# Performance work log

Hardware: AMD Instinct MI355X
Metric: run time of the kernel (lower is better)

## Reference

```python
import jax, jax.numpy as jnp
import numpy as np

CAPACITY_FACTOR = 1.0


def setup_inputs() -> dict:
    key = jax.random.key(0)
    k = jax.random.split(key, 6)
    N, E, M, V = 8192, 8, 1024, 4096
    s = 0.02
    return {
        "x": jax.random.normal(k[0], (N, M), jnp.float32),
        "wg": jax.random.normal(k[1], (E, M), jnp.float32) * s,
        "fc1": jax.random.normal(k[2], (E, M, V), jnp.float32) * s,
        "b1": jax.random.normal(k[3], (E, V), jnp.float32) * s,
        "fc2": jax.random.normal(k[4], (E, V, M), jnp.float32) * s,
        "b2": jax.random.normal(k[5], (E, M), jnp.float32) * s,
    }


def reference(x, wg, fc1, b1, fc2, b2):
    N, M = x.shape
    E = wg.shape[0]
    capacity = 2 * int(CAPACITY_FACTOR * ((N + E - 1) // E))  # Top2 capacity

    # ---- Top2 gating ----
    logits = x @ wg.T                                   # [N, E]
    gates = jax.nn.softmax(logits, axis=1)
    _, top2 = jax.lax.top_k(logits, 2)                  # [N, 2]
    i1, i2 = top2[:, 0], top2[:, 1]
    m1 = jax.nn.one_hot(i1, E, dtype=jnp.int32)         # [N, E]
    m2 = jax.nn.one_hot(i2, E, dtype=jnp.int32)
    g1 = jnp.sum(gates * m1, axis=1)                    # [N]
    g2 = jnp.sum(gates * m2, axis=1)

    # cumulative-sum capacity assignment (per expert slot index)
    loc1 = jnp.cumsum(m1, axis=0) - 1                   # [N, E]
    loc2 = jnp.cumsum(m2, axis=0) - 1 + jnp.sum(m1, axis=0, keepdims=True)
    m1c = m1 * (loc1 < capacity).astype(jnp.int32)
    m2c = m2 * (loc2 < capacity).astype(jnp.int32)
    loc1_s = jnp.sum(loc1 * m1c, axis=1)                # [N]
    loc2_s = jnp.sum(loc2 * m2c, axis=1)
    v1 = jnp.sum(m1c, axis=1)                           # 0/1 kept flags
    v2 = jnp.sum(m2c, axis=1)

    # aux load-balancing loss (fp32 branch of original)
    me = jnp.sum(gates, axis=0)
    ce = jnp.sum(m1c.astype(gates.dtype), axis=0)
    l_aux = jnp.sum(me * ce) * (E / (N * N))

    # ---- dispatch (scatter tokens into [E*C, M]) ----
    idx1 = jnp.where(v1 > 0, i1 * capacity + loc1_s, -1)
    idx2 = jnp.where(v2 > 0, i2 * capacity + loc2_s, -1)
    disp = jnp.zeros((E * capacity, M), x.dtype)
    disp = disp.at[idx1].add(x, mode="drop")
    disp = disp.at[idx2].add(x, mode="drop")

    # ---- fused FFN experts ----
    d = disp.reshape(E, capacity, M)
    h = jnp.einsum("ecm,emv->ecv", d, fc1) + b1[:, None, :]
    h = jax.nn.relu(h)
    y = jnp.einsum("ecv,evm->ecm", h, fc2) + b2[:, None, :]
    yf = y.reshape(E * capacity, M)

    # ---- combine (gather + gate-weighted sum) ----
    v1f = v1.astype(x.dtype)
    v2f = v2.astype(x.dtype)
    out = (g1 * v1f)[:, None] * yf[i1 * capacity + loc1_s] \
        + (g2 * v2f)[:, None] * yf[i2 * capacity + loc2_s]
    return out, l_aux
```

## Files before the change

kernel.cpp:

```cpp
#include <hip/hip_runtime.h>
#include <stdint.h>

typedef __attribute__((ext_vector_type(8))) short short8;
typedef __attribute__((ext_vector_type(4))) float f32x4;

#define N_TOK 8192
#define E_EXP 8
#define M_DIM 1024
#define V_DIM 4096
#define CAP   2048
#define SLOTS (E_EXP*CAP)

__device__ __forceinline__ unsigned short f2bf(float f){
  unsigned u = __float_as_uint(f);
  u += 0x7FFFu + ((u >> 16) & 1u);
  return (unsigned short)(u >> 16);
}

__device__ __forceinline__ void gload_lds16(const void* g, void* l){
  __builtin_amdgcn_global_load_lds(
    (const __attribute__((address_space(1))) void*)g,
    (__attribute__((address_space(3))) void*)l, 16, 0, 0);
}

__global__ __launch_bounds__(256) void routing_kernel(
    const float* __restrict__ x, const float* __restrict__ wg,
    float* __restrict__ gates, int* __restrict__ i1o, int* __restrict__ i2o,
    float* __restrict__ g1o, float* __restrict__ g2o)
{
  int wv = threadIdx.x >> 6, lane = threadIdx.x & 63;
  int n = blockIdx.x * 4 + wv;
  const float* xr = x + (size_t)n * M_DIM;
  double acc[8];
  #pragma unroll
  for (int e = 0; e < 8; e++) acc[e] = 0.0;
  for (int j = 0; j < M_DIM/64; j++){
    double xv = (double)xr[lane + j*64];
    #pragma unroll
    for (int e = 0; e < 8; e++) acc[e] += xv * (double)wg[e*M_DIM + lane + j*64];
  }
  #pragma unroll
  for (int off = 32; off > 0; off >>= 1){
    #pragma unroll
    for (int e = 0; e < 8; e++) acc[e] += __shfl_down(acc[e], off);
  }
  if (lane == 0){
    float lg[8], mx = -1e30f;
    #pragma unroll
    for (int e = 0; e < 8; e++){ lg[e] = (float)acc[e]; mx = fmaxf(mx, lg[e]); }
    float s = 0.f, gt[8];
    #pragma unroll
    for (int e = 0; e < 8; e++){ gt[e] = expf(lg[e] - mx); s += gt[e]; }
    float inv = 1.f / s;
    int i1 = 0;
    #pragma unroll
    for (int e = 1; e < 8; e++) if (lg[e] > lg[i1]) i1 = e;
    int i2 = (i1 == 0) ? 1 : 0;
    #pragma unroll
    for (int e = 0; e < 8; e++){ if (e == i1) continue; if (lg[e] > lg[i2]) i2 = e; }
    #pragma unroll
    for (int e = 0; e < 8; e++) gates[(size_t)n*8 + e] = gt[e] * inv;
    i1o[n] = i1; i2o[n] = i2;
    g1o[n] = gt[i1] * inv; g2o[n] = gt[i2] * inv;
  }
}

__global__ __launch_bounds__(1024) void scan_kernel(
    const int* __restrict__ i1, const int* __restrict__ i2,
    int* __restrict__ s1, int* __restrict__ s2, int* __restrict__ ce_out)
{
  __shared__ unsigned long long sc[4][1024];
  const int t = threadIdx.x;
  int e1l[8], e2l[8];
  unsigned long long c[4] = {0ull,0ull,0ull,0ull};
  #pragma unroll
  for (int k = 0; k < 8; k++){
    int a = i1[t*8+k]; e1l[k] = a; c[a>>2]       += 1ull << ((a&3)*16);
    int b = i2[t*8+k]; e2l[k] = b; c[2 + (b>>2)] += 1ull << ((b&3)*16);
  }
  #pragma unroll
  for (int i = 0; i < 4; i++) sc[i][t] = c[i];
  __syncthreads();
  for (int st = 1; st < 1024; st <<= 1){
    unsigned long long add[4];
    #pragma unroll
    for (int i = 0; i < 4; i++) add[i] = (t >= st) ? sc[i][t-st] : 0ull;
    __syncthreads();
    #pragma unroll
    for (int i = 0; i < 4; i++) if (t >= st) sc[i][t] += add[i];
    __syncthreads();
  }
  unsigned long long ex[4], tot[4];
  #pragma unroll
  for (int i = 0; i < 4; i++){ ex[i] = sc[i][t] - c[i]; tot[i] = sc[i][1023]; }
  int r1[8], r2[8], t1[8];
  #pragma unroll
  for (int e = 0; e < 8; e++){
    r1[e] = (int)((ex[e>>2]       >> ((e&3)*16)) & 0xFFFF);
    r2[e] = (int)((ex[2 + (e>>2)] >> ((e&3)*16)) & 0xFFFF);
    t1[e] = (int)((tot[e>>2]      >> ((e&3)*16)) & 0xFFFF);
  }
  #pragma unroll
  for (int k = 0; k < 8; k++){
    int n = t*8 + k;
    int a = e1l[k]; int loc1 = r1[a]++;
    s1[n] = (loc1 < CAP) ? (a*CAP + loc1) : -1;
    int b = e2l[k]; int loc2 = r2[b]++ + t1[b];
    s2[n] = (loc2 < CAP) ? (b*CAP + loc2) : -1;
  }
  if (t == 0){
    #pragma unroll
    for (int e = 0; e < 8; e++) ce_out[e] = (t1[e] < CAP) ? t1[e] : CAP;
  }
}

__global__ __launch_bounds__(1024) void laux_kernel(
    const float* __restrict__ gates, const int* __restrict__ ce, float* __restrict__ dst)
{
  __shared__ float red[1024];
  const int t = threadIdx.x;
  float part[8];
  #pragma unroll
  for (int e = 0; e < 8; e++) part[e] = 0.f;
  for (int k = 0; k < 8; k++){
    int n = t + k*1024;
    #pragma unroll
    for (int e = 0; e < 8; e++) part[e] += gates[(size_t)n*8 + e];
  }
  float laux = 0.f;
  for (int e = 0; e < 8; e++){
    red[t] = part[e];
    __syncthreads();
    for (int s = 512; s > 0; s >>= 1){ if (t < s) red[t] += red[t+s]; __syncthreads(); }
    if (t == 0) laux += red[0] * (float)ce[e];
    __syncthreads();
  }
  if (t == 0) dst[0] = laux * (float)(8.0/(8192.0*8192.0));
}

__global__ void build_droplist(const int* __restrict__ s1, const int* __restrict__ s2,
                               int* __restrict__ list, int* __restrict__ cnt)
{
  int lane = threadIdx.x;
  int base = 0;
  int a = s1[lane], b = s2[lane];
  for (int it = 0; it < N_TOK/64; it++){
    int na = 0, nb = 0;
    if (it + 1 < N_TOK/64){
      na = s1[(it+1)*64 + lane];
      nb = s2[(it+1)*64 + lane];
    }
    int n = it*64 + lane;
    bool f1 = (a == -1) || (a == SLOTS-1);
    unsigned long long m1 = __ballot(f1);
    if (f1) list[base + __popcll(m1 & ((1ull<<lane)-1))] = n;
    base += __popcll(m1);
    bool f2 = (b == -1) || (b == SLOTS-1);
    unsigned long long m2 = __ballot(f2);
    if (f2) list[base + __popcll(m2 & ((1ull<<lane)-1))] = n;
    base += __popcll(m2);
    a = na; b = nb;
  }
  if (lane == 0) *cnt = base;
}

__global__ void dropacc1_kernel(const float* __restrict__ x, const int* __restrict__ list,
                                const int* __restrict__ cnt, float* __restrict__ partial)
{
  int col = blockIdx.x*256 + threadIdx.x;
  int sl  = blockIdx.y;
  int c = *cnt;
  int per = (c + 15) >> 4;
  int lo = sl*per, hi = lo + per; if (hi > c) hi = c;
  float a = 0.f;
  for (int i = lo; i < hi; i++) a += x[(size_t)list[i]*M_DIM + col];
  partial[sl*M_DIM + col] = a;
}
__global__ void dropacc2_kernel(const float* __restrict__ partial, float* __restrict__ drow)
{
  int col = blockIdx.x*256 + threadIdx.x;
  float s = 0.f;
  #pragma unroll
  for (int j = 0; j < 16; j++) s += partial[j*M_DIM + col];
  drow[col] = s;
}

template<bool RELU>
__global__ __launch_bounds__(256) void fix_gemv(
    const float* __restrict__ vec, const float* __restrict__ W,
    const float* __restrict__ bias, float* __restrict__ outv, int K, int N)
{
  __shared__ float red[256];
  const int o = threadIdx.x & 15;
  const int c = threadIdx.x >> 4;
  const int n = blockIdx.x*16 + o;
  const int chunk = K >> 4;
  float a = 0.f;
  for (int k = c*chunk; k < (c+1)*chunk; k++) a += vec[k] * W[(size_t)k*N + n];
  red[threadIdx.x] = a;
  __syncthreads();
  if (c == 0){
    float s = 0.f;
    #pragma unroll
    for (int j = 0; j < 16; j++) s += red[o + j*16];
    s += bias[n];
    if (RELU) s = fmaxf(s, 0.f);
    outv[n] = s;
  }
}

__global__ void scatter_kernel(const float* __restrict__ x, const int* __restrict__ s1,
                               const int* __restrict__ s2, unsigned short* __restrict__ dispB,
                               int e0, int epb)
{
  int n = blockIdx.x, t = threadIdx.x;
  int a = s1[n], b = s2[n];
  int za = (a >= 0) ? (a >> 11) - e0 : -1;
  int zb = (b >= 0) ? (b >> 11) - e0 : -1;
  bool wa = (za >= 0) && (za < epb);
  bool wb = (zb >= 0) && (zb < epb);
  if (!wa && !wb) return;
  const float4 v = *(const float4*)(x + (size_t)n*M_DIM + t*4);
  ushort4 o;
  o.x = f2bf(v.x); o.y = f2bf(v.y); o.z = f2bf(v.z); o.w = f2bf(v.w);
  if (wa) *(ushort4*)(dispB + ((size_t)za*CAP + (a & (CAP-1)))*M_DIM + t*4) = o;
  if (wb) *(ushort4*)(dispB + ((size_t)zb*CAP + (b & (CAP-1)))*M_DIM + t*4) = o;
}

__global__ __launch_bounds__(256) void transpose_f32_bf16(
    const float* __restrict__ in, unsigned short* __restrict__ out,
    int R, int C, size_t estride)
{
  __shared__ float tile[32][33];
  const size_t eo = (size_t)blockIdx.z * estride;
  int c0 = blockIdx.x*32, r0 = blockIdx.y*32;
  int tx = threadIdx.x & 31, ty = threadIdx.x >> 5;
  #pragma unroll
  for (int j = 0; j < 4; j++)
    tile[ty + j*8][tx] = in[eo + (size_t)(r0 + ty + j*8)*C + (c0 + tx)];
  __syncthreads();
  #pragma unroll
  for (int j = 0; j < 4; j++)
    out[eo + (size_t)(c0 + ty + j*8)*R + (r0 + tx)] = f2bf(tile[tx][ty + j*8]);
}

template<bool RELU_BF16>
__global__ __launch_bounds__(512, 2) void gemm_tn(
    const unsigned short* __restrict__ A, size_t aE,
    const unsigned short* __restrict__ B, size_t bE,
    const float* __restrict__ bias, size_t biasE,
    void* __restrict__ outp, size_t oE, int K, int Ncols, int gx, int gy)
{
  __shared__ unsigned short As[2][2][128*64];
  __shared__ unsigned short Bs[2][2][128*64];
  const int nwg = gridDim.x;
  const int orig = blockIdx.x;
  const int wgid = (orig & 7) * (nwg >> 3) + (orig >> 3);
  const int z  = wgid / (gx*gy);
  const int rr = wgid - z*gx*gy;
  const int by = rr / gx, bx = rr - by*gx;

  const unsigned short* Ae = A + (size_t)z * aE;
  const unsigned short* Be = B + (size_t)z * bE;
  const float* be = bias + (size_t)z * biasE;
  const int row0 = by * 256;
  const int col0 = bx * 256;
  const int tid = threadIdx.x;
  const int lane = tid & 63, wv = tid >> 6;
  const int wr = wv >> 2, wc = wv & 3;
  const int frow = lane & 15, fq = lane >> 4;

  f32x4 acc[8][4];
  #pragma unroll
  for (int i = 0; i < 8; i++)
    #pragma unroll
    for (int j = 0; j < 4; j++) acc[i][j] = (f32x4){0.f,0.f,0.f,0.f};

  auto STAGE_A = [&](int buf, int half, int k0){
    #pragma unroll
    for (int i = 0; i < 2; i++){
      int cb = i*512 + wv*64;
      int c  = cb + lane;
      int r  = c >> 3, s = c & 7;
      gload_lds16(Ae + (size_t)(row0 + half*128 + r)*K + (k0 + ((s ^ (r & 7))*8)),
                  &As[buf][half][cb*8]);
    }
  };
  auto STAGE_B = [&](int buf, int half, int k0){
    #pragma unroll
    for (int i = 0; i < 2; i++){
      int cb = i*512 + wv*64;
      int c  = cb + lane;
      int r  = c >> 3, s = c & 7;
      gload_lds16(Be + (size_t)(col0 + half*128 + r)*K + (k0 + ((s ^ (r & 7))*8)),
                  &Bs[buf][half][cb*8]);
    }
  };

  short8 a[8], bA[4], bB[4];
  auto READ_A = [&](int buf, int fmb){
    #pragma unroll
    for (int fm = 0; fm < 4; fm++)
      #pragma unroll
      for (int ks = 0; ks < 2; ks++){
        int row = wr*128 + (fmb+fm)*16 + frow;
        int h = row >> 7, r = row & 127;
        int sl = (ks*4 + fq) ^ (r & 7);
        a[fm*2+ks] = *(const short8*)&As[buf][h][r*64 + sl*8];
      }
  };
  auto READ_B = [&](int buf, int fnb, short8* dst){
    #pragma unroll
    for (int fn = 0; fn < 2; fn++)
      #pragma unroll
      for (int ks = 0; ks < 2; ks++){
        int col = wc*64 + (fnb+fn)*16 + frow;
        int h = col >> 7, r = col & 127;
        int sl = (ks*4 + fq) ^ (r & 7);
        dst[fn*2+ks] = *(const short8*)&Bs[buf][h][r*64 + sl*8];
      }
  };
  auto MFMA16 = [&](int fmb, int fnb, short8* b){
    #pragma unroll
    for (int fm = 0; fm < 4; fm++)
      #pragma unroll
      for (int fn = 0; fn < 2; fn++)
        #pragma unroll
        for (int ks = 0; ks < 2; ks++)
          acc[fmb+fm][fnb+fn] =
            __builtin_amdgcn_mfma_f32_16x16x32_bf16(a[fm*2+ks], b[fn*2+ks], acc[fmb+fm][fnb+fn], 0, 0, 0);
  };

  const int nt = K >> 6;
  const int iters = nt >> 1;
  STAGE_A(0, 0, 0); STAGE_A(0, 1, 0);
  STAGE_B(0, 0, 0); STAGE_B(0, 1, 0);
  STAGE_B(1, 0, 64); STAGE_B(1, 1, 64);
  asm volatile("s_waitcnt vmcnt(4)" ::: "memory");
  __builtin_amdgcn_sched_barrier(0);
  __builtin_amdgcn_s_barrier();

  for (int t = 0; t < iters; ++t){
    const bool more = (t + 1 < iters);
    const int kO = (2*t+1)*64;
    const int kN = (2*t+2)*64;
    const int kL = (2*t+3)*64;

    READ_A(0, 0); READ_B(0, 0, bA);
    STAGE_A(1, 0, kO);
    __builtin_amdgcn_s_barrier();
    asm volatile("s_waitcnt lgkmcnt(0)" ::: "memory");
    __builtin_amdgcn_sched_barrier(0);
    __builtin_amdgcn_s_setprio(1); MFMA16(0, 0, bA); __builtin_amdgcn_s_setprio(0);
    __builtin_amdgcn_s_barrier();
    READ_B(0, 2, bB);
    STAGE_A(1, 1, kO);
    __builtin_amdgcn_s_barrier();
    asm volatile("s_waitcnt lgkmcnt(0)" ::: "memory");
    __builtin_amdgcn_sched_barrier(0);
    __builtin_amdgcn_s_setprio(1); MFMA16(0, 2, bB); __builtin_amdgcn_s_setprio(0);
    __builtin_amdgcn_s_barrier();
    READ_A(0, 4);
    if (more) STAGE_B(0, 0, kN);
    __builtin_amdgcn_s_barrier();
    asm volatile("s_waitcnt lgkmcnt(0)" ::: "memory");
    __builtin_amdgcn_sched_barrier(0);
    __builtin_amdgcn_s_setprio(1); MFMA16(4, 0, bA); __builtin_amdgcn_s_setprio(0);
    __builtin_amdgcn_s_barrier();
    if (more) STAGE_B(0, 1, kN);
    __builtin_amdgcn_s_barrier();
    asm volatile("s_waitcnt lgkmcnt(0)" ::: "memory");
    __builtin_amdgcn_sched_barrier(0);
    __builtin_amdgcn_s_setprio(1); MFMA16(4, 2, bB); __builtin_amdgcn_s_setprio(0);
    if (more) asm volatile("s_waitcnt vmcnt(4)" ::: "memory");
    else      asm volatile("s_waitcnt vmcnt(0)" ::: "memory");
    __builtin_amdgcn_sched_barrier(0);
    __builtin_amdgcn_s_barrier();

    READ_A(1, 0); READ_B(1, 0, bA);
    if (more) STAGE_A(0, 0, kN);
    __builtin_amdgcn_s_barrier();
    asm volatile("s_waitcnt lgkmcnt(0)" ::: "memory");
    __builtin_amdgcn_sched_barrier(0);
    __builtin_amdgcn_s_setprio(1); MFMA16(0, 0, bA); __builtin_amdgcn_s_setprio(0);
    __builtin_amdgcn_s_barrier();
    READ_B(1, 2, bB);
    if (more) STAGE_A(0, 1, kN);
    __builtin_amdgcn_s_barrier();
    asm volatile("s_waitcnt lgkmcnt(0)" ::: "memory");
    __builtin_amdgcn_sched_barrier(0);
    __builtin_amdgcn_s_setprio(1); MFMA16(0, 2, bB); __builtin_amdgcn_s_setprio(0);
    __builtin_amdgcn_s_barrier();
    READ_A(1, 4);
    if (more) STAGE_B(1, 0, kL);
    __builtin_amdgcn_s_barrier();
    asm volatile("s_waitcnt lgkmcnt(0)" ::: "memory");
    __builtin_amdgcn_sched_barrier(0);
    __builtin_amdgcn_s_setprio(1); MFMA16(4, 0, bA); __builtin_amdgcn_s_setprio(0);
    __builtin_amdgcn_s_barrier();
    if (more) STAGE_B(1, 1, kL);
    __builtin_amdgcn_s_barrier();
    asm volatile("s_waitcnt lgkmcnt(0)" ::: "memory");
    __builtin_amdgcn_sched_barrier(0);
    __builtin_amdgcn_s_setprio(1); MFMA16(4, 2, bB); __builtin_amdgcn_s_setprio(0);
    if (more){
      asm volatile("s_waitcnt vmcnt(4)" ::: "memory");
      __builtin_amdgcn_sched_barrier(0);
    }
    __builtin_amdgcn_s_barrier();
  }

  const int rsub = fq * 4;
  #pragma unroll
  for (int fn = 0; fn < 4; fn++){
    int col = col0 + wc*64 + fn*16 + frow;
    float bv = be[col];
    #pragma unroll
    for (int fm = 0; fm < 8; fm++){
      int row = row0 + wr*128 + fm*16 + rsub;
      #pragma unroll
      for (int r = 0; r < 4; r++){
        float v = acc[fm][fn][r] + bv;
        if (RELU_BF16){
          v = fmaxf(v, 0.f);
          ((unsigned short*)outp)[(size_t)z*oE + (size_t)(row + r)*Ncols + col] = f2bf(v);
        } else {
          ((float*)outp)[(size_t)z*oE + (size_t)(row + r)*Ncols + col] = v;
        }
      }
    }
  }
}

__global__ void gather_full_kernel(const float* __restrict__ y, const int* __restrict__ s1,
    const int* __restrict__ s2, const float* __restrict__ g1, const float* __restrict__ g2,
    float* __restrict__ out)
{
  int n = blockIdx.x, t = threadIdx.x;
  int a = s1[n], b = s2[n];
  float c1 = (a >= 0) ? g1[n] : 0.f; int p1 = (a >= 0) ? a : 0;
  float c2 = (b >= 0) ? g2[n] : 0.f; int p2 = (b >= 0) ? b : 0;
  const float4 v1 = *(const float4*)(y + (size_t)p1*M_DIM + t*4);
  const float4 v2 = *(const float4*)(y + (size_t)p2*M_DIM + t*4);
  float4 o;
  o.x = c1*v1.x + c2*v2.x; o.y = c1*v1.y + c2*v2.y;
  o.z = c1*v1.z + c2*v2.z; o.w = c1*v1.w + c2*v2.w;
  *(float4*)(out + (size_t)n*M_DIM + t*4) = o;
}

__global__ void gather_kernel(const float* __restrict__ yB, const int* __restrict__ s1,
    const int* __restrict__ s2, const float* __restrict__ g1, const float* __restrict__ g2,
    float* __restrict__ out, int e0, int epb)
{
  int n = blockIdx.x, t = threadIdx.x;
  int a = s1[n], b = s2[n];
  float4 o;
  bool touched = false;
  for (int z = 0; z < epb; z++){
    int e = e0 + z;
    float coef = 0.f; int loc = 0; bool m = false;
    if (a >= 0 && (a >> 11) == e){ coef = g1[n]; loc = a & (CAP-1); m = true; }
    else if (b >= 0 && (b >> 11) == e){ coef = g2[n]; loc = b & (CAP-1); m = true; }
    if (m){
      if (!touched) o = *(const float4*)(out + (size_t)n*M_DIM + t*4);
      const float4 v = *(const float4*)(yB + ((size_t)z*CAP + loc)*M_DIM + t*4);
      o.x += coef*v.x; o.y += coef*v.y; o.z += coef*v.z; o.w += coef*v.w;
      touched = true;
    }
  }
  if (touched) *(float4*)(out + (size_t)n*M_DIM + t*4) = o;
}

extern "C" void kernel_launch(void* const* d_in, const int* in_sizes, int n_in,
                              void* d_out, int out_size, void* d_ws, size_t ws_size,
                              hipStream_t stream)
{
  const float* x   = (const float*)d_in[0];
  const float* wg  = (const float*)d_in[1];
  const float* fc1 = (const float*)d_in[2];
  const float* b1  = (const float*)d_in[3];
  const float* fc2 = (const float*)d_in[4];
  const float* b2  = (const float*)d_in[5];
  float* out = (float*)d_out;
  char* ws = (char*)d_ws;

  size_t off = 0;
  auto take = [&](size_t b)->char*{ char* p = ws + off; off += (b + 255) & ~(size_t)255; return p; };

  float* gates = (float*)take((size_t)N_TOK*8*4);
  int*   i1    = (int*)  take((size_t)N_TOK*4);
  int*   i2    = (int*)  take((size_t)N_TOK*4);
  float* g1    = (float*)take((size_t)N_TOK*4);
  float* g2    = (float*)take((size_t)N_TOK*4);
  int*   s1    = (int*)  take((size_t)N_TOK*4);
  int*   s2    = (int*)  take((size_t)N_TOK*4);
  int*   ce    = (int*)  take(256);
  int*   list  = (int*)  take((size_t)2*N_TOK*4);
  int*   cnt   = (int*)  take(256);
  float* dpart = (float*)take((size_t)16*M_DIM*4);
  float* drow  = (float*)take((size_t)M_DIM*4);
  float* hrow  = (float*)take((size_t)V_DIM*4);

  const size_t perExp = (size_t)CAP*M_DIM*2
                      + (size_t)M_DIM*V_DIM*2*2
                      + (size_t)CAP*V_DIM*2
                      + (size_t)CAP*M_DIM*4;
  int epb = 0;
  {
    const int cands[3] = {8, 4, 2};
    for (int ci = 0; ci < 3; ci++){
      if (off + (size_t)cands[ci]*perExp + (1u<<20) <= ws_size){ epb = cands[ci]; break; }
    }
  }
  if (!epb){
    hipMemsetAsync(d_out, 0, (size_t)out_size*4, stream);
    return;
  }
  unsigned short* dispB = (unsigned short*)take((size_t)epb*CAP*M_DIM*2);
  unsigned short* fc1bB = (unsigned short*)take((size_t)epb*M_DIM*V_DIM*2);
  unsigned short* fc2bB = (unsigned short*)take((size_t)epb*M_DIM*V_DIM*2);
  unsigned short* hB    = (unsigned short*)take((size_t)epb*CAP*V_DIM*2);
  float*          yB    = (float*)         take((size_t)epb*CAP*M_DIM*4);

  routing_kernel<<<N_TOK/4, 256, 0, stream>>>(x, wg, gates, i1, i2, g1, g2);
  scan_kernel<<<1, 1024, 0, stream>>>(i1, i2, s1, s2, ce);
  laux_kernel<<<1, 1024, 0, stream>>>(gates, ce, out + (size_t)N_TOK*M_DIM);
  if (epb < 8) hipMemsetAsync(out, 0, (size_t)N_TOK*M_DIM*4, stream);
  build_droplist<<<1, 64, 0, stream>>>(s1, s2, list, cnt);
  dropacc1_kernel<<<dim3(4,16), 256, 0, stream>>>(x, list, cnt, dpart);
  dropacc2_kernel<<<4, 256, 0, stream>>>(dpart, drow);

  const size_t eW = (size_t)M_DIM*V_DIM;
  for (int e0 = 0; e0 < E_EXP; e0 += epb){
    scatter_kernel<<<N_TOK, 256, 0, stream>>>(x, s1, s2, dispB, e0, epb);
    transpose_f32_bf16<<<dim3(V_DIM/32, M_DIM/32, epb), 256, 0, stream>>>(fc1 + (size_t)e0*eW, fc1bB, M_DIM, V_DIM, eW);
    transpose_f32_bf16<<<dim3(M_DIM/32, V_DIM/32, epb), 256, 0, stream>>>(fc2 + (size_t)e0*eW, fc2bB, V_DIM, M_DIM, eW);
    gemm_tn<true ><<<(V_DIM/256)*(CAP/256)*epb, 512, 0, stream>>>(
        dispB, (size_t)CAP*M_DIM, fc1bB, eW, b1 + (size_t)e0*V_DIM, V_DIM,
        hB, (size_t)CAP*V_DIM, M_DIM, V_DIM, V_DIM/256, CAP/256);
    gemm_tn<false><<<(M_DIM/256)*(CAP/256)*epb, 512, 0, stream>>>(
        hB, (size_t)CAP*V_DIM, fc2bB, eW, b2 + (size_t)e0*M_DIM, M_DIM,
        yB, (size_t)CAP*M_DIM, V_DIM, M_DIM, M_DIM/256, CAP/256);
    if (E_EXP-1 >= e0 && E_EXP-1 < e0+epb){
      fix_gemv<true ><<<V_DIM/16, 256, 0, stream>>>(drow, fc1 + (size_t)(E_EXP-1)*eW, b1 + (size_t)(E_EXP-1)*V_DIM, hrow, M_DIM, V_DIM);
      fix_gemv<false><<<M_DIM/16, 256, 0, stream>>>(hrow, fc2 + (size_t)(E_EXP-1)*eW, b2 + (size_t)(E_EXP-1)*M_DIM,
                                                    yB + ((size_t)(E_EXP-1-e0)*CAP + (CAP-1))*M_DIM, V_DIM, M_DIM);
    }
    if (epb < 8)
      gather_kernel<<<N_TOK, 256, 0, stream>>>(yB, s1, s2, g1, g2, out, e0, epb);
  }
  if (epb == 8)
    gather_full_kernel<<<N_TOK, 256, 0, stream>>>(yB, s1, s2, g1, g2, out);
}
```

Before: 669.1 us.

## Fuse token dispatch into first GEMM via slot-to-token indirection and stage epilogue through LDS

Removes the scatter kernel and the dispatch buffer. The first GEMM now reads bf16 token rows straight from a pre-converted copy of x, using a slot-to-token table, with empty slots pointing at a zero row. Precomputed per-thread A/B row pointers simplify the staging address math. Both GEMM epilogues are restaged through LDS so global stores are wide and coalesced, at the cost of extra barriers and LDS traffic. Converting all of x to bf16 adds a full pass over the input, and the gathered A loads are less regular.

```diff
diff --git a/kernel.cpp b/kernel.cpp
--- a/kernel.cpp
+++ b/kernel.cpp
@@ -209,22 +209,27 @@
   }
 }
 
-__global__ void scatter_kernel(const float* __restrict__ x, const int* __restrict__ s1,
-                               const int* __restrict__ s2, unsigned short* __restrict__ dispB,
-                               int e0, int epb)
-{
-  int n = blockIdx.x, t = threadIdx.x;
+__global__ __launch_bounds__(256) void convert_x_kernel(
+    const float* __restrict__ x, unsigned short* __restrict__ xb)
+{
+  size_t i = ((size_t)blockIdx.x*256 + threadIdx.x) * 8;
+  float4 f0 = *(const float4*)(x + i);
+  float4 f1 = *(const float4*)(x + i + 4);
+  short8 v;
+  v[0] = (short)f2bf(f0.x); v[1] = (short)f2bf(f0.y);
+  v[2] = (short)f2bf(f0.z); v[3] = (short)f2bf(f0.w);
+  v[4] = (short)f2bf(f1.x); v[5] = (short)f2bf(f1.y);
+  v[6] = (short)f2bf(f1.z); v[7] = (short)f2bf(f1.w);
+  *(short8*)(xb + i) = v;
+}
+
+__global__ void tok_fill_kernel(const int* __restrict__ s1, const int* __restrict__ s2,
+                                int* __restrict__ tok)
+{
+  int n = blockIdx.x*256 + threadIdx.x;
   int a = s1[n], b = s2[n];
-  int za = (a >= 0) ? (a >> 11) - e0 : -1;
-  int zb = (b >= 0) ? (b >> 11) - e0 : -1;
-  bool wa = (za >= 0) && (za < epb);
-  bool wb = (zb >= 0) && (zb < epb);
-  if (!wa && !wb) return;
-  const float4 v = *(const float4*)(x + (size_t)n*M_DIM + t*4);
-  ushort4 o;
-  o.x = f2bf(v.x); o.y = f2bf(v.y); o.z = f2bf(v.z); o.w = f2bf(v.w);
-  if (wa) *(ushort4*)(dispB + ((size_t)za*CAP + (a & (CAP-1)))*M_DIM + t*4) = o;
-  if (wb) *(ushort4*)(dispB + ((size_t)zb*CAP + (b & (CAP-1)))*M_DIM + t*4) = o;
+  if (a >= 0) tok[a] = n;
+  if (b >= 0) tok[b] = n;
 }
 
 __global__ __launch_bounds__(256) void transpose_f32_bf16(
@@ -244,15 +249,18 @@
     out[eo + (size_t)(c0 + ty + j*8)*R + (r0 + tx)] = f2bf(tile[tx][ty + j*8]);
 }
 
-template<bool RELU_BF16>
+template<bool RELU_BF16, bool AIND>
 __global__ __launch_bounds__(512, 2) void gemm_tn(
     const unsigned short* __restrict__ A, size_t aE,
     const unsigned short* __restrict__ B, size_t bE,
     const float* __restrict__ bias, size_t biasE,
-    void* __restrict__ outp, size_t oE, int K, int Ncols, int gx, int gy)
-{
-  __shared__ unsigned short As[2][2][128*64];
-  __shared__ unsigned short Bs[2][2][128*64];
+    void* __restrict__ outp, size_t oE, int K, int Ncols, int gx, int gy,
+    const int* __restrict__ tok, const unsigned short* __restrict__ xb,
+    const unsigned short* __restrict__ zrow, int slotbase)
+{
+  __shared__ unsigned short SH[65536];
+  auto As = reinterpret_cast<unsigned short(*)[2][128*64]>(SH);
+  auto Bs = reinterpret_cast<unsigned short(*)[2][128*64]>(SH + 32768);
   const int nwg = gridDim.x;
   const int orig = blockIdx.x;
   const int wgid = (orig & 7) * (nwg >> 3) + (orig >> 3);
@@ -260,7 +268,6 @@
   const int rr = wgid - z*gx*gy;
   const int by = rr / gx, bx = rr - by*gx;
 
-  const unsigned short* Ae = A + (size_t)z * aE;
   const unsigned short* Be = B + (size_t)z * bE;
   const float* be = bias + (size_t)z * biasE;
   const int row0 = by * 256;
@@ -270,6 +277,24 @@
   const int wr = wv >> 2, wc = wv & 3;
   const int frow = lane & 15, fq = lane >> 4;
 
+  const int rbase = (wv*64 + lane) >> 3;
+  const int swz   = (((lane & 7) ^ (rbase & 7)) * 8);
+  const unsigned short* pA[2][2];
+  const unsigned short* pB[2][2];
+  #pragma unroll
+  for (int h = 0; h < 2; h++)
+    #pragma unroll
+    for (int i = 0; i < 2; i++){
+      int gr = row0 + h*128 + rbase + i*64;
+      if (AIND){
+        int tk = tok[slotbase + z*CAP + gr];
+        pA[h][i] = (tk < 0) ? zrow : (xb + (size_t)tk * M_DIM);
+      } else {
+        pA[h][i] = A + (size_t)z * aE + (size_t)gr * K;
+      }
+      pB[h][i] = Be + (size_t)(col0 + h*128 + rbase + i*64) * K;
+    }
+
   f32x4 acc[8][4];
   #pragma unroll
   for (int i = 0; i < 8; i++)
@@ -278,23 +303,13 @@
 
   auto STAGE_A = [&](int buf, int half, int k0){
     #pragma unroll
-    for (int i = 0; i < 2; i++){
-      int cb = i*512 + wv*64;
-      int c  = cb + lane;
-      int r  = c >> 3, s = c & 7;
-      gload_lds16(Ae + (size_t)(row0 + half*128 + r)*K + (k0 + ((s ^ (r & 7))*8)),
-                  &As[buf][half][cb*8]);
-    }
+    for (int i = 0; i < 2; i++)
+      gload_lds16(pA[half][i] + k0 + swz, &As[buf][half][(i*512 + wv*64)*8]);
   };
   auto STAGE_B = [&](int buf, int half, int k0){
     #pragma unroll
-    for (int i = 0; i < 2; i++){
-      int cb = i*512 + wv*64;
-      int c  = cb + lane;
-      int r  = c >> 3, s = c & 7;
-      gload_lds16(Be + (size_t)(col0 + half*128 + r)*K + (k0 + ((s ^ (r & 7))*8)),
-                  &Bs[buf][half][cb*8]);
-    }
+    for (int i = 0; i < 2; i++)
+      gload_lds16(pB[half][i] + k0 + swz, &Bs[buf][half][(i*512 + wv*64)*8]);
   };
 
   short8 a[8], bA[4], bB[4];
@@ -411,23 +426,55 @@
   }
 
   const int rsub = fq * 4;
-  #pragma unroll
-  for (int fn = 0; fn < 4; fn++){
-    int col = col0 + wc*64 + fn*16 + frow;
-    float bv = be[col];
-    #pragma unroll
-    for (int fm = 0; fm < 8; fm++){
-      int row = row0 + wr*128 + fm*16 + rsub;
+  if (RELU_BF16){
+    unsigned short* ep = SH;
+    #pragma unroll
+    for (int fn = 0; fn < 4; fn++){
+      int col = wc*64 + fn*16 + frow;
+      float bv = be[col0 + col];
       #pragma unroll
-      for (int r = 0; r < 4; r++){
-        float v = acc[fm][fn][r] + bv;
-        if (RELU_BF16){
-          v = fmaxf(v, 0.f);
-          ((unsigned short*)outp)[(size_t)z*oE + (size_t)(row + r)*Ncols + col] = f2bf(v);
-        } else {
-          ((float*)outp)[(size_t)z*oE + (size_t)(row + r)*Ncols + col] = v;
+      for (int fm = 0; fm < 8; fm++){
+        int row = wr*128 + fm*16 + rsub;
+        #pragma unroll
+        for (int r = 0; r < 4; r++)
+          ep[(row + r)*256 + col] = f2bf(fmaxf(acc[fm][fn][r] + bv, 0.f));
+      }
+    }
+    __builtin_amdgcn_s_barrier();
+    unsigned short* hp = (unsigned short*)outp + (size_t)z*oE;
+    #pragma unroll
+    for (int j = 0; j < 16; j++){
+      int chunk = tid + j*512;
+      int row = chunk >> 5, off = (chunk & 31)*8;
+      *(short8*)(hp + (size_t)(row0 + row)*Ncols + col0 + off) = *(const short8*)&ep[row*256 + off];
+    }
+  } else {
+    float* ep32 = (float*)SH;
+    float* yp = (float*)outp + (size_t)z*oE;
+    #pragma unroll
+    for (int ph = 0; ph < 2; ph++){
+      if (wr == ph){
+        #pragma unroll
+        for (int fn = 0; fn < 4; fn++){
+          int col = wc*64 + fn*16 + frow;
+          float bv = be[col0 + col];
+          #pragma unroll
+          for (int fm = 0; fm < 8; fm++){
+            int rloc = fm*16 + rsub;
+            #pragma unroll
+            for (int r = 0; r < 4; r++)
+              ep32[(rloc + r)*256 + col] = acc[fm][fn][r] + bv;
+          }
         }
       }
+      __builtin_amdgcn_s_barrier();
+      #pragma unroll
+      for (int j = 0; j < 16; j++){
+        int chunk = tid + j*512;
+        int rloc = chunk >> 6, off = (chunk & 63)*4;
+        *(f32x4*)(yp + (size_t)(row0 + ph*128 + rloc)*Ncols + col0 + off) = *(const f32x4*)&ep32[rloc*256 + off];
+      }
+      __builtin_amdgcn_s_barrier();
     }
   }
 }
@@ -500,9 +547,11 @@
   float* dpart = (float*)take((size_t)16*M_DIM*4);
   float* drow  = (float*)take((size_t)M_DIM*4);
   float* hrow  = (float*)take((size_t)V_DIM*4);
-
-  const size_t perExp = (size_t)CAP*M_DIM*2
-                      + (size_t)M_DIM*V_DIM*2*2
+  unsigned short* xb   = (unsigned short*)take((size_t)N_TOK*M_DIM*2);
+  int*            tok  = (int*)           take((size_t)SLOTS*4);
+  unsigned short* zrow = (unsigned short*)take((size_t)M_DIM*2);
+
+  const size_t perExp = (size_t)M_DIM*V_DIM*2*2
                       + (size_t)CAP*V_DIM*2
                       + (size_t)CAP*M_DIM*4;
   int epb = 0;
@@ -516,7 +565,6 @@
     hipMemsetAsync(d_out, 0, (size_t)out_size*4, stream);
     return;
   }
-  unsigned short* dispB = (unsigned short*)take((size_t)epb*CAP*M_DIM*2);
   unsigned short* fc1bB = (unsigned short*)take((size_t)epb*M_DIM*V_DIM*2);
   unsigned short* fc2bB = (unsigned short*)take((size_t)epb*M_DIM*V_DIM*2);
   unsigned short* hB    = (unsigned short*)take((size_t)epb*CAP*V_DIM*2);
@@ -526,21 +574,26 @@
   scan_kernel<<<1, 1024, 0, stream>>>(i1, i2, s1, s2, ce);
   laux_kernel<<<1, 1024, 0, stream>>>(gates, ce, out + (size_t)N_TOK*M_DIM);
   if (epb < 8) hipMemsetAsync(out, 0, (size_t)N_TOK*M_DIM*4, stream);
+  hipMemsetAsync(tok, 0xFF, (size_t)SLOTS*4, stream);
+  hipMemsetAsync(zrow, 0, (size_t)M_DIM*2, stream);
+  tok_fill_kernel<<<N_TOK/256, 256, 0, stream>>>(s1, s2, tok);
+  convert_x_kernel<<<(N_TOK*M_DIM)/(256*8), 256, 0, stream>>>(x, xb);
   build_droplist<<<1, 64, 0, stream>>>(s1, s2, list, cnt);
   dropacc1_kernel<<<dim3(4,16), 256, 0, stream>>>(x, list, cnt, dpart);
   dropacc2_kernel<<<4, 256, 0, stream>>>(dpart, drow);
 
   const size_t eW = (size_t)M_DIM*V_DIM;
   for (int e0 = 0; e0 < E_EXP; e0 += epb){
-    scatter_kernel<<<N_TOK, 256, 0, stream>>>(x, s1, s2, dispB, e0, epb);
     transpose_f32_bf16<<<dim3(V_DIM/32, M_DIM/32, epb), 256, 0, stream>>>(fc1 + (size_t)e0*eW, fc1bB, M_DIM, V_DIM, eW);
     transpose_f32_bf16<<<dim3(M_DIM/32, V_DIM/32, epb), 256, 0, stream>>>(fc2 + (size_t)e0*eW, fc2bB, V_DIM, M_DIM, eW);
-    gemm_tn<true ><<<(V_DIM/256)*(CAP/256)*epb, 512, 0, stream>>>(
-        dispB, (size_t)CAP*M_DIM, fc1bB, eW, b1 + (size_t)e0*V_DIM, V_DIM,
-        hB, (size_t)CAP*V_DIM, M_DIM, V_DIM, V_DIM/256, CAP/256);
-    gemm_tn<false><<<(M_DIM/256)*(CAP/256)*epb, 512, 0, stream>>>(
+    gemm_tn<true, true><<<(V_DIM/256)*(CAP/256)*epb, 512, 0, stream>>>(
+        nullptr, 0, fc1bB, eW, b1 + (size_t)e0*V_DIM, V_DIM,
+        hB, (size_t)CAP*V_DIM, M_DIM, V_DIM, V_DIM/256, CAP/256,
+        tok, xb, zrow, e0*CAP);
+    gemm_tn<false, false><<<(M_DIM/256)*(CAP/256)*epb, 512, 0, stream>>>(
         hB, (size_t)CAP*V_DIM, fc2bB, eW, b2 + (size_t)e0*M_DIM, M_DIM,
-        yB, (size_t)CAP*M_DIM, V_DIM, M_DIM, M_DIM/256, CAP/256);
+        yB, (size_t)CAP*M_DIM, V_DIM, M_DIM, M_DIM/256, CAP/256,
+        nullptr, nullptr, nullptr, 0);
     if (E_EXP-1 >= e0 && E_EXP-1 < e0+epb){
       fix_gemv<true ><<<V_DIM/16, 256, 0, stream>>>(drow, fc1 + (size_t)(E_EXP-1)*eW, b1 + (size_t)(E_EXP-1)*V_DIM, hrow, M_DIM, V_DIM);
       fix_gemv<false><<<M_DIM/16, 256, 0, stream>>>(hrow, fc2 + (size_t)(E_EXP-1)*eW, b2 + (size_t)(E_EXP-1)*M_DIM,
```

Measured after the change: 591.1 us. 1.13x faster.
